# Optimization experiments

Measured on AMD Instinct MI355X. Metric: run time of the kernel, lower is better.

Reference implementation:

```python
import jax, jax.numpy as jnp
import numpy as np

B, S, D = 2, 2048, 1024
H = 16
HD = D // H

def setup_inputs() -> dict:
    key = jax.random.key(0)
    ks = jax.random.split(key, 9)
    s = 1.0 / np.sqrt(D)
    return {
        "x": jax.random.normal(ks[0], (B, S, D), dtype=jnp.float32),
        "Wq": jax.random.normal(ks[1], (D, D), dtype=jnp.float32) * s,
        "bq": jnp.zeros((D,), dtype=jnp.float32),
        "Wk": jax.random.normal(ks[2], (D, D), dtype=jnp.float32) * s,
        "bk": jnp.zeros((D,), dtype=jnp.float32),
        "Wv": jax.random.normal(ks[3], (D, D), dtype=jnp.float32) * s,
        "bv": jnp.zeros((D,), dtype=jnp.float32),
        "Wo": jax.random.normal(ks[4], (D, D), dtype=jnp.float32) * s,
        "bo": jnp.zeros((D,), dtype=jnp.float32),
    }

def reference(x, Wq, bq, Wk, bk, Wv, bv, Wo, bo):
    b, s, d = x.shape
    # torch Linear: y = x @ W.T + b
    def proj(W, bias):
        y = jnp.einsum('bsd,ed->bse', x, W) + bias
        return y.reshape(b, s, H, HD).transpose(0, 2, 1, 3)  # [b,h,s,hd]
    Q = proj(Wq, bq)
    K = proj(Wk, bk)
    V = proj(Wv, bv)
    scale = 1.0 / jnp.sqrt(jnp.float32(HD))
    scores = jnp.einsum('bhqd,bhkd->bhqk', Q, K) * scale  # [b,h,s,s]
    attn = jax.nn.softmax(scores, axis=-1)
    out = jnp.einsum('bhqk,bhkd->bhqd', attn, V)  # [b,h,s,hd]
    out = out.transpose(0, 2, 1, 3).reshape(b, s, d)
    return jnp.einsum('bsd,ed->bse', out, Wo) + bo
```

## Files before the change

### kernel.cpp

```cpp
#include <hip/hip_runtime.h>
#include <stdint.h>


typedef __bf16 bf16x8 __attribute__((ext_vector_type(8)));
typedef __bf16 bf16x4 __attribute__((ext_vector_type(4)));
typedef float  f32x4  __attribute__((ext_vector_type(4)));
typedef unsigned short u16x4 __attribute__((ext_vector_type(4)));

#define LOG2E 1.44269504088896f
#define FIXED_MAX_BITS 14.4269504088896f

__device__ __forceinline__ unsigned short f2bf(float f) {
    union { float f; unsigned u; } v; v.f = f;
    unsigned r = v.u + 0x7FFFu + ((v.u >> 16) & 1u);
    return (unsigned short)(r >> 16);
}

__device__ __forceinline__ float exp2_fast(float x) {
#if __has_builtin(__builtin_amdgcn_exp2f)
    return __builtin_amdgcn_exp2f(x);
#else
    return __expf(x * 0.69314718056f);
#endif
}

__device__ __forceinline__ f32x4 pv_mfma(bf16x4 v, bf16x4 p, f32x4 c) {
#if __has_builtin(__builtin_amdgcn_mfma_f32_16x16x16_bf16)
    return __builtin_amdgcn_mfma_f32_16x16x16_bf16(v, p, c, 0, 0, 0);
#elif __has_builtin(__builtin_amdgcn_mfma_f32_16x16x16bf16_1k)
    typedef short s16x4 __attribute__((ext_vector_type(4)));
    return __builtin_amdgcn_mfma_f32_16x16x16bf16_1k(
        __builtin_bit_cast(s16x4, v), __builtin_bit_cast(s16x4, p), c, 0, 0, 0);
#else
    const bf16x4 z = {(__bf16)0.f, (__bf16)0.f, (__bf16)0.f, (__bf16)0.f};
    bf16x8 v8 = __builtin_shufflevector(v, z, 0, 1, 2, 3, 4, 5, 6, 7);
    bf16x8 p8 = __builtin_shufflevector(p, z, 0, 1, 2, 3, 4, 5, 6, 7);
    return __builtin_amdgcn_mfma_f32_16x16x32_bf16(v8, p8, c, 0, 0, 0);
#endif
}

__device__ __forceinline__ void glds16(const void* g, void* l) {
    __builtin_amdgcn_global_load_lds(
        (__attribute__((address_space(1))) void*)(g),
        (__attribute__((address_space(3))) void*)(l),
        16, 0, 0);
}

__global__ __launch_bounds__(256) void cvt_all(
    const float* __restrict__ x,  const float* __restrict__ Wq,
    const float* __restrict__ Wk, const float* __restrict__ Wv,
    const float* __restrict__ Wo,
    unsigned short* __restrict__ xb,  unsigned short* __restrict__ Wqb,
    unsigned short* __restrict__ Wkb, unsigned short* __restrict__ Wvb,
    unsigned short* __restrict__ Wob)
{
    const int stride = gridDim.x * blockDim.x;
    for (int i = blockIdx.x * blockDim.x + threadIdx.x; i < 2097152; i += stride) {
        const float* src; unsigned short* dst; int j;
        if (i < 1048576) { src = x; dst = xb; j = i; }
        else {
            int t = (i - 1048576) >> 18; j = (i - 1048576) & 262143;
            src = (t == 0) ? Wq : (t == 1) ? Wk : (t == 2) ? Wv : Wo;
            dst = (t == 0) ? Wqb : (t == 1) ? Wkb : (t == 2) ? Wvb : Wob;
        }
        float4 v = ((const float4*)src)[j];
        ushort4 o;
        o.x = f2bf(v.x); o.y = f2bf(v.y); o.z = f2bf(v.z); o.w = f2bf(v.w);
        ((ushort4*)dst)[j] = o;
    }
}

template <int MODE>
__global__ __launch_bounds__(256) void gemm_bt(
    const unsigned short* __restrict__ A,
    const unsigned short* __restrict__ W0,
    const unsigned short* __restrict__ W1,
    const unsigned short* __restrict__ W2,
    const float* __restrict__ b0,
    const float* __restrict__ b1,
    const float* __restrict__ b2,
    unsigned short* __restrict__ outQ,
    unsigned short* __restrict__ outK,
    unsigned short* __restrict__ outV,
    float* __restrict__ outF)
{
    constexpr int BM = (MODE == 0) ? 128 : 64;
    constexpr int FM = BM / 32;
    constexpr int RA = BM / 32;

    __shared__ __attribute__((aligned(16))) unsigned short As[BM * 64];
    __shared__ __attribute__((aligned(16))) unsigned short Bs[128 * 64];

    const int tid  = threadIdx.x;
    const int lane = tid & 63;
    const int wid  = tid >> 6;
    const int quad = lane >> 4;
    const int l16  = lane & 15;

    const int m0 = blockIdx.x * BM;

    const unsigned short* W;
    const float* bias;
    int proj, n0;
    if (MODE == 0) {
        proj = blockIdx.y >> 3;
        n0   = (blockIdx.y & 7) * 128;
        W    = (proj == 0) ? W0 : (proj == 1) ? W1 : W2;
        bias = (proj == 0) ? b0 : (proj == 1) ? b1 : b2;
    } else {
        proj = 0;
        n0   = blockIdx.y * 128;
        W    = W0;
        bias = b0;
    }

    const int wm = (wid >> 1) * (BM / 2);
    const int wn = (wid & 1) * 64;

    f32x4 acc[FM][4];
#pragma unroll
    for (int i = 0; i < FM; ++i)
#pragma unroll
        for (int j = 0; j < 4; ++j)
            acc[i][j] = (f32x4){0.f, 0.f, 0.f, 0.f};

    char* AsB  = (char*)As;
    char* BsB  = (char*)Bs;
    char* ldsA = AsB + wid * 1024;
    char* ldsB = BsB + wid * 1024;

    for (int k0 = 0; k0 < 1024; k0 += 64) {
#pragma unroll
        for (int q = 0; q < RA; ++q) {
            int i   = q * 256 + tid;
            int row = i >> 3;
            int sc  = (i & 7) ^ (row & 7);
            glds16(A + (size_t)(m0 + row) * 1024 + k0 + sc * 8, ldsA + q * 4096);
        }
#pragma unroll
        for (int q = 0; q < 4; ++q) {
            int i   = q * 256 + tid;
            int row = i >> 3;
            int sc  = (i & 7) ^ (row & 7);
            glds16(W + (size_t)(n0 + row) * 1024 + k0 + sc * 8, ldsB + q * 4096);
        }
        __syncthreads();

#pragma unroll
        for (int kh = 0; kh < 2; ++kh) {
            bf16x8 af[FM], bfr[4];
#pragma unroll
            for (int t = 0; t < FM; ++t) {
                int r = wm + t * 16 + l16;
                int c = (kh * 4 + quad) ^ (r & 7);
                af[t] = *(const bf16x8*)(AsB + r * 128 + c * 16);
            }
#pragma unroll
            for (int t = 0; t < 4; ++t) {
                int r = wn + t * 16 + l16;
                int c = (kh * 4 + quad) ^ (r & 7);
                bfr[t] = *(const bf16x8*)(BsB + r * 128 + c * 16);
            }
#pragma unroll
            for (int i = 0; i < FM; ++i)
#pragma unroll
                for (int j = 0; j < 4; ++j)
                    acc[i][j] = __builtin_amdgcn_mfma_f32_16x16x32_bf16(
                        af[i], bfr[j], acc[i][j], 0, 0, 0);
        }
        __syncthreads();
    }

#pragma unroll
    for (int i = 0; i < FM; ++i) {
        const int mrow0 = m0 + wm + i * 16 + quad * 4;
#pragma unroll
        for (int j = 0; j < 4; ++j) {
            const int n  = n0 + wn + j * 16 + l16;
            const float bb = bias[n];
            if (MODE == 1) {
#pragma unroll
                for (int r = 0; r < 4; ++r)
                    outF[(size_t)(mrow0 + r) * 1024 + n] = acc[i][j][r] + bb;
            } else {
                const int h = n >> 6, hd = n & 63;
                if (proj == 2) {
                    const int b = mrow0 >> 11, s = mrow0 & 2047;
                    ushort4 pk;
                    pk.x = f2bf(acc[i][j][0] + bb);
                    pk.y = f2bf(acc[i][j][1] + bb);
                    pk.z = f2bf(acc[i][j][2] + bb);
                    pk.w = f2bf(acc[i][j][3] + bb);
                    *(ushort4*)(outV + ((size_t)((b * 16 + h) * 64 + hd)) * 2048 + s) = pk;
                } else {
                    unsigned short* dst = (proj == 0) ? outQ : outK;
                    const float scl = (proj == 0) ? (0.125f * LOG2E) : 1.0f;
#pragma unroll
                    for (int r = 0; r < 4; ++r) {
                        const int m = mrow0 + r;
                        const int b = m >> 11, s = m & 2047;
                        dst[((size_t)((b * 16 + h) * 2048 + s)) * 64 + hd] =
                            f2bf((acc[i][j][r] + bb) * scl);
                    }
                }
            }
        }
    }
}

__global__ __launch_bounds__(256) void attn_kernel(
    const unsigned short* __restrict__ Qb,
    const unsigned short* __restrict__ Kb,
    const unsigned short* __restrict__ Vtb,
    unsigned short* __restrict__ Ob)
{
    __shared__ __attribute__((aligned(16))) unsigned short Ks[128 * 64];
    __shared__ __attribute__((aligned(16))) unsigned short Vs[2 * 64 * 64];

    const int tid  = threadIdx.x;
    const int lane = tid & 63;
    const int wid  = tid >> 6;
    const int quad = lane >> 4;
    const int l16  = lane & 15;

    const int q0 = blockIdx.x * 128 + wid * 32;
    const int hb = blockIdx.y;
    const int bq = hb >> 4, hh = hb & 15;

    const unsigned short* Qh  = Qb  + (size_t)hb * 2048 * 64;
    const unsigned short* Kh  = Kb  + (size_t)hb * 2048 * 64;
    const unsigned short* Vth = Vtb + (size_t)hb * 64 * 2048;

    bf16x8 qf[2][2];
#pragma unroll
    for (int qt = 0; qt < 2; ++qt) {
        const unsigned short* qp = Qh + (size_t)(q0 + qt * 16 + l16) * 64 + quad * 8;
        qf[qt][0] = *(const bf16x8*)(qp);
        qf[qt][1] = *(const bf16x8*)(qp + 32);
    }

    f32x4 o[4][2];
#pragma unroll
    for (int ht = 0; ht < 4; ++ht)
#pragma unroll
        for (int qt = 0; qt < 2; ++qt)
            o[ht][qt] = (f32x4){0.f, 0.f, 0.f, 0.f};
    float lsum[2] = {0.f, 0.f};

    char* KsB = (char*)Ks;
    char* ldsK = KsB + wid * 1024;

    const int l7  = l16 & 7;
    const int kb0 = l16 * 128 + ((quad) ^ l7) * 16;
    const int kb1 = l16 * 128 + ((4 + quad) ^ l7) * 16;
    int vb[4];
#pragma unroll
    for (int t = 0; t < 4; ++t)
        vb[t] = l16 * 128 + (((t * 2 + (quad >> 1)) ^ l7) * 16) + (quad & 1) * 8;

    for (int kc = 0; kc < 2048; kc += 128) {
#pragma unroll
        for (int q = 0; q < 4; ++q) {
            int i   = q * 256 + tid;
            int row = i >> 3;
            int sc  = (i & 7) ^ (row & 7);
            glds16(Kh + (size_t)(kc + row) * 64 + sc * 8, ldsK + q * 4096);
        }
#pragma unroll
        for (int sub = 0; sub < 2; ++sub)
#pragma unroll
            for (int q = 0; q < 2; ++q) {
                int i   = q * 256 + tid;
                int row = i >> 3;
                int sc  = (i & 7) ^ (row & 7);
                glds16(Vth + (size_t)row * 2048 + kc + sub * 64 + sc * 8,
                       (char*)Vs + sub * 8192 + wid * 1024 + q * 4096);
            }
        __syncthreads();

#pragma unroll
        for (int st = 0; st < 8; ++st) {
            const bf16x8 k0 = *(const bf16x8*)(KsB + st * 2048 + kb0);
            const bf16x8 k1 = *(const bf16x8*)(KsB + st * 2048 + kb1);

            bf16x4 pb[2];
#pragma unroll
            for (int qt = 0; qt < 2; ++qt) {
                f32x4 s = (f32x4){-FIXED_MAX_BITS, -FIXED_MAX_BITS,
                                  -FIXED_MAX_BITS, -FIXED_MAX_BITS};
                s = __builtin_amdgcn_mfma_f32_16x16x32_bf16(k0, qf[qt][0], s, 0, 0, 0);
                s = __builtin_amdgcn_mfma_f32_16x16x32_bf16(k1, qf[qt][1], s, 0, 0, 0);
                float p0 = exp2_fast(s[0]);
                float p1 = exp2_fast(s[1]);
                float p2 = exp2_fast(s[2]);
                float p3 = exp2_fast(s[3]);
                lsum[qt] += (p0 + p1) + (p2 + p3);
                u16x4 up;
                up.x = f2bf(p0); up.y = f2bf(p1);
                up.z = f2bf(p2); up.w = f2bf(p3);
                pb[qt] = __builtin_bit_cast(bf16x4, up);
            }

            const int ssoff = (st >> 2) * 8192;
            const int tl    = st & 3;
#pragma unroll
            for (int ht = 0; ht < 4; ++ht) {
                const bf16x4 vf = *(const bf16x4*)
                    ((char*)Vs + ssoff + ht * 2048 + vb[tl]);
                o[ht][0] = pv_mfma(vf, pb[0], o[ht][0]);
                o[ht][1] = pv_mfma(vf, pb[1], o[ht][1]);
            }
        }
        __syncthreads();
    }

    float rl[2];
#pragma unroll
    for (int qt = 0; qt < 2; ++qt) {
        float s = lsum[qt];
        s += __shfl_xor(s, 16);
        s += __shfl_xor(s, 32);
        rl[qt] = 1.0f / s;
    }

#pragma unroll
    for (int qt = 0; qt < 2; ++qt) {
        const size_t row = (size_t)(bq * 2048 + q0 + qt * 16 + l16);
#pragma unroll
        for (int ht = 0; ht < 4; ++ht) {
            ushort4 pk;
            pk.x = f2bf(o[ht][qt][0] * rl[qt]);
            pk.y = f2bf(o[ht][qt][1] * rl[qt]);
            pk.z = f2bf(o[ht][qt][2] * rl[qt]);
            pk.w = f2bf(o[ht][qt][3] * rl[qt]);
            *(ushort4*)(Ob + row * 1024 + hh * 64 + ht * 16 + quad * 4) = pk;
        }
    }
}

extern "C" void kernel_launch(void* const* d_in, const int* in_sizes, int n_in,
                              void* d_out, int out_size, void* d_ws, size_t ws_size,
                              hipStream_t stream) {
    (void)in_sizes; (void)n_in; (void)out_size; (void)ws_size;

    const float* x  = (const float*)d_in[0];
    const float* Wq = (const float*)d_in[1];
    const float* bq = (const float*)d_in[2];
    const float* Wk = (const float*)d_in[3];
    const float* bk = (const float*)d_in[4];
    const float* Wv = (const float*)d_in[5];
    const float* bv = (const float*)d_in[6];
    const float* Wo = (const float*)d_in[7];
    const float* bo = (const float*)d_in[8];

    char* ws = (char*)d_ws;
    const size_t MB = 1024 * 1024;
    unsigned short* xb    = (unsigned short*)(ws + 0);
    unsigned short* Wqb   = (unsigned short*)(ws + 8  * MB);
    unsigned short* Wkb   = (unsigned short*)(ws + 10 * MB);
    unsigned short* Wvb   = (unsigned short*)(ws + 12 * MB);
    unsigned short* Wob   = (unsigned short*)(ws + 14 * MB);
    unsigned short* Qb    = (unsigned short*)(ws + 16 * MB);
    unsigned short* Kb    = (unsigned short*)(ws + 24 * MB);
    unsigned short* Vtb   = (unsigned short*)(ws + 32 * MB);
    unsigned short* attnb = (unsigned short*)(ws + 40 * MB);

    cvt_all<<<dim3(1024), dim3(256), 0, stream>>>(
        x, Wq, Wk, Wv, Wo, xb, Wqb, Wkb, Wvb, Wob);

    gemm_bt<0><<<dim3(32, 24), dim3(256), 0, stream>>>(
        xb, Wqb, Wkb, Wvb, bq, bk, bv, Qb, Kb, Vtb, nullptr);

    attn_kernel<<<dim3(16, 32), dim3(256), 0, stream>>>(Qb, Kb, Vtb, attnb);

    gemm_bt<1><<<dim3(64, 8), dim3(256), 0, stream>>>(
        attnb, Wob, nullptr, nullptr, bo, nullptr, nullptr,
        nullptr, nullptr, nullptr, (float*)d_out);
}
```

Measured before the change: 208.6 us.

## Split attention over key halves and switch PV to 16x16x32 MFMA

Splits each attention block's key range in two (split-K), doubling the grid to 1024 blocks. The unnormalized partial outputs go to a bf16 workspace and the row sums to a float buffer. A new reduce kernel adds the two halves and normalizes them. The inner loop now processes 32 keys per step, uses a re-swizzled K layout, and runs PV on 16x16x32 MFMAs with 8-wide P fragments instead of 16x16x16 ones. It also adds an occupancy hint of 4 blocks per CU. The aim is better CU fill and MFMA efficiency, at the cost of an extra kernel launch, extra memory traffic, and bf16 rounding of the partial outputs.

```diff
diff --git a/kernel.cpp b/kernel.cpp
--- a/kernel.cpp
+++ b/kernel.cpp
@@ -3,9 +3,8 @@
 
 
 typedef __bf16 bf16x8 __attribute__((ext_vector_type(8)));
-typedef __bf16 bf16x4 __attribute__((ext_vector_type(4)));
 typedef float  f32x4  __attribute__((ext_vector_type(4)));
-typedef unsigned short u16x4 __attribute__((ext_vector_type(4)));
+typedef unsigned short u16x8 __attribute__((ext_vector_type(8)));
 
 #define LOG2E 1.44269504088896f
 #define FIXED_MAX_BITS 14.4269504088896f
@@ -14,6 +13,9 @@
     union { float f; unsigned u; } v; v.f = f;
     unsigned r = v.u + 0x7FFFu + ((v.u >> 16) & 1u);
     return (unsigned short)(r >> 16);
+}
+__device__ __forceinline__ float bf2f(unsigned short u) {
+    union { unsigned u; float f; } v; v.u = (unsigned)u << 16; return v.f;
 }
 
 __device__ __forceinline__ float exp2_fast(float x) {
@@ -21,21 +23,6 @@
     return __builtin_amdgcn_exp2f(x);
 #else
     return __expf(x * 0.69314718056f);
-#endif
-}
-
-__device__ __forceinline__ f32x4 pv_mfma(bf16x4 v, bf16x4 p, f32x4 c) {
-#if __has_builtin(__builtin_amdgcn_mfma_f32_16x16x16_bf16)
-    return __builtin_amdgcn_mfma_f32_16x16x16_bf16(v, p, c, 0, 0, 0);
-#elif __has_builtin(__builtin_amdgcn_mfma_f32_16x16x16bf16_1k)
-    typedef short s16x4 __attribute__((ext_vector_type(4)));
-    return __builtin_amdgcn_mfma_f32_16x16x16bf16_1k(
-        __builtin_bit_cast(s16x4, v), __builtin_bit_cast(s16x4, p), c, 0, 0, 0);
-#else
-    const bf16x4 z = {(__bf16)0.f, (__bf16)0.f, (__bf16)0.f, (__bf16)0.f};
-    bf16x8 v8 = __builtin_shufflevector(v, z, 0, 1, 2, 3, 4, 5, 6, 7);
-    bf16x8 p8 = __builtin_shufflevector(p, z, 0, 1, 2, 3, 4, 5, 6, 7);
-    return __builtin_amdgcn_mfma_f32_16x16x32_bf16(v8, p8, c, 0, 0, 0);
 #endif
 }
 
@@ -208,11 +195,12 @@
     }
 }
 
-__global__ __launch_bounds__(256) void attn_kernel(
+__global__ __launch_bounds__(256, 4) void attn_kernel(
     const unsigned short* __restrict__ Qb,
     const unsigned short* __restrict__ Kb,
     const unsigned short* __restrict__ Vtb,
-    unsigned short* __restrict__ Ob)
+    unsigned short* __restrict__ OP,
+    float* __restrict__ LS)
 {
     __shared__ __attribute__((aligned(16))) unsigned short Ks[128 * 64];
     __shared__ __attribute__((aligned(16))) unsigned short Vs[2 * 64 * 64];
@@ -222,10 +210,12 @@
     const int wid  = tid >> 6;
     const int quad = lane >> 4;
     const int l16  = lane & 15;
-
-    const int q0 = blockIdx.x * 128 + wid * 32;
-    const int hb = blockIdx.y;
-    const int bq = hb >> 4, hh = hb & 15;
+    const int l7   = l16 & 7;
+
+    const int half = blockIdx.x & 1;
+    const int q0   = (blockIdx.x >> 1) * 128 + wid * 32;
+    const int hb   = blockIdx.y;
+    const int bq   = hb >> 4, hh = hb & 15;
 
     const unsigned short* Qh  = Qb  + (size_t)hb * 2048 * 64;
     const unsigned short* Kh  = Kb  + (size_t)hb * 2048 * 64;
@@ -247,24 +237,23 @@
             o[ht][qt] = (f32x4){0.f, 0.f, 0.f, 0.f};
     float lsum[2] = {0.f, 0.f};
 
-    char* KsB = (char*)Ks;
+    char* KsB  = (char*)Ks;
     char* ldsK = KsB + wid * 1024;
 
-    const int l7  = l16 & 7;
-    const int kb0 = l16 * 128 + ((quad) ^ l7) * 16;
-    const int kb1 = l16 * 128 + ((4 + quad) ^ l7) * 16;
-    int vb[4];
-#pragma unroll
-    for (int t = 0; t < 4; ++t)
-        vb[t] = l16 * 128 + (((t * 2 + (quad >> 1)) ^ l7) * 16) + (quad & 1) * 8;
-
-    for (int kc = 0; kc < 2048; kc += 128) {
+    const int base_row = 8 * (l16 >> 2) + (l16 & 3);
+    const int kp0 = ((quad) ^ l7) * 16;
+    const int kp1 = ((4 + quad) ^ l7) * 16;
+    const int vrow = l16 * 128;
+
+    const int kc0 = half * 1024;
+    for (int kc = kc0; kc < kc0 + 1024; kc += 128) {
 #pragma unroll
         for (int q = 0; q < 4; ++q) {
             int i   = q * 256 + tid;
             int row = i >> 3;
-            int sc  = (i & 7) ^ (row & 7);
-            glds16(Kh + (size_t)(kc + row) * 64 + sc * 8, ldsK + q * 4096);
+            int g   = (row & 3) | (((row >> 3) & 1) << 2);
+            int ch  = (i & 7) ^ g;
+            glds16(Kh + (size_t)(kc + row) * 64 + ch * 8, ldsK + q * 4096);
         }
 #pragma unroll
         for (int sub = 0; sub < 2; ++sub)
@@ -272,70 +261,117 @@
             for (int q = 0; q < 2; ++q) {
                 int i   = q * 256 + tid;
                 int row = i >> 3;
-                int sc  = (i & 7) ^ (row & 7);
-                glds16(Vth + (size_t)row * 2048 + kc + sub * 64 + sc * 8,
+                int ch  = (i & 7) ^ (row & 7);
+                glds16(Vth + (size_t)row * 2048 + kc + sub * 64 + ch * 8,
                        (char*)Vs + sub * 8192 + wid * 1024 + q * 4096);
             }
         __syncthreads();
 
 #pragma unroll
-        for (int st = 0; st < 8; ++st) {
-            const bf16x8 k0 = *(const bf16x8*)(KsB + st * 2048 + kb0);
-            const bf16x8 k1 = *(const bf16x8*)(KsB + st * 2048 + kb1);
-
-            bf16x4 pb[2];
+        for (int st32 = 0; st32 < 4; ++st32) {
+            const char* krb = KsB + (st32 * 32 + base_row) * 128;
+            bf16x8 kf00 = *(const bf16x8*)(krb + kp0);
+            bf16x8 kf01 = *(const bf16x8*)(krb + kp1);
+            bf16x8 kf10 = *(const bf16x8*)(krb + 512 + kp0);
+            bf16x8 kf11 = *(const bf16x8*)(krb + 512 + kp1);
+
+            const f32x4 mi = (f32x4){-FIXED_MAX_BITS, -FIXED_MAX_BITS,
+                                     -FIXED_MAX_BITS, -FIXED_MAX_BITS};
+            f32x4 s00 = mi, s01 = mi, s10 = mi, s11 = mi;
+            s00 = __builtin_amdgcn_mfma_f32_16x16x32_bf16(kf00, qf[0][0], s00, 0, 0, 0);
+            s00 = __builtin_amdgcn_mfma_f32_16x16x32_bf16(kf01, qf[0][1], s00, 0, 0, 0);
+            s01 = __builtin_amdgcn_mfma_f32_16x16x32_bf16(kf10, qf[0][0], s01, 0, 0, 0);
+            s01 = __builtin_amdgcn_mfma_f32_16x16x32_bf16(kf11, qf[0][1], s01, 0, 0, 0);
+            s10 = __builtin_amdgcn_mfma_f32_16x16x32_bf16(kf00, qf[1][0], s10, 0, 0, 0);
+            s10 = __builtin_amdgcn_mfma_f32_16x16x32_bf16(kf01, qf[1][1], s10, 0, 0, 0);
+            s11 = __builtin_amdgcn_mfma_f32_16x16x32_bf16(kf10, qf[1][0], s11, 0, 0, 0);
+            s11 = __builtin_amdgcn_mfma_f32_16x16x32_bf16(kf11, qf[1][1], s11, 0, 0, 0);
+
+            bf16x8 p8[2];
 #pragma unroll
             for (int qt = 0; qt < 2; ++qt) {
-                f32x4 s = (f32x4){-FIXED_MAX_BITS, -FIXED_MAX_BITS,
-                                  -FIXED_MAX_BITS, -FIXED_MAX_BITS};
-                s = __builtin_amdgcn_mfma_f32_16x16x32_bf16(k0, qf[qt][0], s, 0, 0, 0);
-                s = __builtin_amdgcn_mfma_f32_16x16x32_bf16(k1, qf[qt][1], s, 0, 0, 0);
-                float p0 = exp2_fast(s[0]);
-                float p1 = exp2_fast(s[1]);
-                float p2 = exp2_fast(s[2]);
-                float p3 = exp2_fast(s[3]);
-                lsum[qt] += (p0 + p1) + (p2 + p3);
-                u16x4 up;
-                up.x = f2bf(p0); up.y = f2bf(p1);
-                up.z = f2bf(p2); up.w = f2bf(p3);
-                pb[qt] = __builtin_bit_cast(bf16x4, up);
-            }
-
-            const int ssoff = (st >> 2) * 8192;
-            const int tl    = st & 3;
+                const f32x4 sA = qt ? s10 : s00;
+                const f32x4 sB = qt ? s11 : s01;
+                float e0 = exp2_fast(sA[0]), e1 = exp2_fast(sA[1]);
+                float e2 = exp2_fast(sA[2]), e3 = exp2_fast(sA[3]);
+                float e4 = exp2_fast(sB[0]), e5 = exp2_fast(sB[1]);
+                float e6 = exp2_fast(sB[2]), e7 = exp2_fast(sB[3]);
+                lsum[qt] += ((e0 + e1) + (e2 + e3)) + ((e4 + e5) + (e6 + e7));
+                u16x8 up;
+                up[0] = f2bf(e0); up[1] = f2bf(e1); up[2] = f2bf(e2); up[3] = f2bf(e3);
+                up[4] = f2bf(e4); up[5] = f2bf(e5); up[6] = f2bf(e6); up[7] = f2bf(e7);
+                p8[qt] = __builtin_bit_cast(bf16x8, up);
+            }
+
+            const int voff = (st32 >> 1) * 8192 + vrow
+                           + ((((st32 & 1) * 4 + quad) ^ l7) * 16);
 #pragma unroll
             for (int ht = 0; ht < 4; ++ht) {
-                const bf16x4 vf = *(const bf16x4*)
-                    ((char*)Vs + ssoff + ht * 2048 + vb[tl]);
-                o[ht][0] = pv_mfma(vf, pb[0], o[ht][0]);
-                o[ht][1] = pv_mfma(vf, pb[1], o[ht][1]);
+                const bf16x8 vf = *(const bf16x8*)((char*)Vs + voff + ht * 2048);
+                o[ht][0] = __builtin_amdgcn_mfma_f32_16x16x32_bf16(vf, p8[0], o[ht][0], 0, 0, 0);
+                o[ht][1] = __builtin_amdgcn_mfma_f32_16x16x32_bf16(vf, p8[1], o[ht][1], 0, 0, 0);
             }
         }
         __syncthreads();
     }
 
-    float rl[2];
+    float lt[2];
 #pragma unroll
     for (int qt = 0; qt < 2; ++qt) {
         float s = lsum[qt];
         s += __shfl_xor(s, 16);
         s += __shfl_xor(s, 32);
-        rl[qt] = 1.0f / s;
-    }
-
+        lt[qt] = s;
+    }
+
+    unsigned short* OPh = OP + (size_t)half * 4096 * 1024;
 #pragma unroll
     for (int qt = 0; qt < 2; ++qt) {
         const size_t row = (size_t)(bq * 2048 + q0 + qt * 16 + l16);
 #pragma unroll
         for (int ht = 0; ht < 4; ++ht) {
             ushort4 pk;
-            pk.x = f2bf(o[ht][qt][0] * rl[qt]);
-            pk.y = f2bf(o[ht][qt][1] * rl[qt]);
-            pk.z = f2bf(o[ht][qt][2] * rl[qt]);
-            pk.w = f2bf(o[ht][qt][3] * rl[qt]);
-            *(ushort4*)(Ob + row * 1024 + hh * 64 + ht * 16 + quad * 4) = pk;
-        }
-    }
+            pk.x = f2bf(o[ht][qt][0]);
+            pk.y = f2bf(o[ht][qt][1]);
+            pk.z = f2bf(o[ht][qt][2]);
+            pk.w = f2bf(o[ht][qt][3]);
+            *(ushort4*)(OPh + row * 1024 + hh * 64 + ht * 16 + quad * 4) = pk;
+        }
+    }
+    if (quad == 0) {
+        LS[half * 65536 + hb * 2048 + q0 + l16]      = lt[0];
+        LS[half * 65536 + hb * 2048 + q0 + 16 + l16] = lt[1];
+    }
+}
+
+__global__ __launch_bounds__(256) void attn_reduce(
+    const unsigned short* __restrict__ OP,
+    const float* __restrict__ LS,
+    unsigned short* __restrict__ attnb)
+{
+    const size_t idx = ((size_t)blockIdx.x * 256 + threadIdx.x) * 8;
+    const int row = (int)(idx >> 10);
+    const int col = (int)(idx & 1023);
+    const int bh  = ((row >> 11) << 4) + (col >> 6);
+    const int q   = row & 2047;
+    const float l = LS[bh * 2048 + q] + LS[65536 + bh * 2048 + q];
+    const float rl = 1.0f / l;
+
+    ushort4 a0 = *(const ushort4*)(OP + idx);
+    ushort4 a1 = *(const ushort4*)(OP + idx + 4);
+    ushort4 b0 = *(const ushort4*)(OP + 4194304 + idx);
+    ushort4 b1 = *(const ushort4*)(OP + 4194304 + idx + 4);
+    ushort4 o0, o1;
+    o0.x = f2bf((bf2f(a0.x) + bf2f(b0.x)) * rl);
+    o0.y = f2bf((bf2f(a0.y) + bf2f(b0.y)) * rl);
+    o0.z = f2bf((bf2f(a0.z) + bf2f(b0.z)) * rl);
+    o0.w = f2bf((bf2f(a0.w) + bf2f(b0.w)) * rl);
+    o1.x = f2bf((bf2f(a1.x) + bf2f(b1.x)) * rl);
+    o1.y = f2bf((bf2f(a1.y) + bf2f(b1.y)) * rl);
+    o1.z = f2bf((bf2f(a1.z) + bf2f(b1.z)) * rl);
+    o1.w = f2bf((bf2f(a1.w) + bf2f(b1.w)) * rl);
+    *(ushort4*)(attnb + idx)     = o0;
+    *(ushort4*)(attnb + idx + 4) = o1;
 }
 
 extern "C" void kernel_launch(void* const* d_in, const int* in_sizes, int n_in,
@@ -364,6 +400,8 @@
     unsigned short* Kb    = (unsigned short*)(ws + 24 * MB);
     unsigned short* Vtb   = (unsigned short*)(ws + 32 * MB);
     unsigned short* attnb = (unsigned short*)(ws + 40 * MB);
+    unsigned short* OP    = (unsigned short*)(ws + 48 * MB);
+    float*          LSb   = (float*)(ws + 64 * MB);
 
     cvt_all<<<dim3(1024), dim3(256), 0, stream>>>(
         x, Wq, Wk, Wv, Wo, xb, Wqb, Wkb, Wvb, Wob);
@@ -371,7 +409,9 @@
     gemm_bt<0><<<dim3(32, 24), dim3(256), 0, stream>>>(
         xb, Wqb, Wkb, Wvb, bq, bk, bv, Qb, Kb, Vtb, nullptr);
 
-    attn_kernel<<<dim3(16, 32), dim3(256), 0, stream>>>(Qb, Kb, Vtb, attnb);
+    attn_kernel<<<dim3(32, 32), dim3(256), 0, stream>>>(Qb, Kb, Vtb, OP, LSb);
+
+    attn_reduce<<<dim3(2048), dim3(256), 0, stream>>>(OP, LSb, attnb);
 
     gemm_bt<1><<<dim3(64, 8), dim3(256), 0, stream>>>(
         attnb, Wob, nullptr, nullptr, bo, nullptr, nullptr,
```

New measurement: 199.1 us. -4.5%, faster.
